# Optimization experiments

Hardware: AMD Instinct MI355X
Metric: run time of the kernel (lower is better)

## Reference

```python
import jax, jax.numpy as jnp
import numpy as np

V = 4096      # num codes (vocab)
D = 128       # embedding dim
K = 3         # diffusion scales
H = 4         # attn heads
FF = 128      # ff hidden
L = 2         # attn layers
NVIS = 8192   # visits
MAXC = 32     # max codes per visit
PAD = 0


def logmap0(x):
    # Poincare ball (c=1) log map at origin: artanh(||x||) * x / ||x||
    eps = 1e-7
    norm = jnp.linalg.norm(x, axis=-1, keepdims=True)
    norm_c = jnp.clip(norm, eps, 1.0 - 1e-5)
    return jnp.arctanh(norm_c) * x / jnp.maximum(norm, eps)


def layer_norm(x, g, b, eps=1e-5):
    m = jnp.mean(x, axis=-1, keepdims=True)
    v = jnp.mean((x - m) ** 2, axis=-1, keepdims=True)
    return (x - m) * jax.lax.rsqrt(v + eps) * g + b


def attn_block(x, Wqkv, bqkv, Wo, bo, W1, b1, W2, b2, g1, be1, g2, be2):
    # x: [V, D] (batch of 1, squeezed)
    hd = D // H
    qkv = x @ Wqkv.T + bqkv                      # [V, 3D]
    q, k, v = jnp.split(qkv, 3, axis=-1)
    q = q.reshape(V, H, hd)
    k = k.reshape(V, H, hd)
    v = v.reshape(V, H, hd)
    scores = jnp.einsum('shd,thd->hst', q, k) / np.sqrt(hd).astype(x.dtype)
    a = jax.nn.softmax(scores, axis=-1)          # [H, V, V]
    o = jnp.einsum('hst,thd->shd', a, v).reshape(V, D)
    attn_out = o @ Wo.T + bo
    x = layer_norm(x + attn_out, g1, be1)
    ff = jax.nn.gelu(x @ W1.T + b1) @ W2.T + b2
    return layer_norm(x + ff, g2, be2)


def setup_inputs() -> dict:
    key = jax.random.key(0)
    ks = jax.random.split(key, 20)
    inp = {}
    inp['visits'] = jax.random.randint(ks[0], (NVIS, MAXC), 0, V)
    # hyperbolic points inside unit ball
    inp['X_hyp'] = jax.random.normal(ks[1], (V, D), jnp.float32) * 0.01
    inp['kernels'] = jax.random.normal(ks[2], (K, V, V), jnp.float32) / V
    inp['proj_W'] = jax.random.normal(ks[3], (D, K * D), jnp.float32) * 0.05
    inp['proj_b'] = jnp.zeros((D,), jnp.float32)
    s = 0.05
    inp['Wqkv'] = jax.random.normal(ks[4], (L, 3 * D, D), jnp.float32) * s
    inp['bqkv'] = jnp.zeros((L, 3 * D), jnp.float32)
    inp['Wo'] = jax.random.normal(ks[5], (L, D, D), jnp.float32) * s
    inp['bo'] = jnp.zeros((L, D), jnp.float32)
    inp['W1'] = jax.random.normal(ks[6], (L, FF, D), jnp.float32) * s
    inp['b1'] = jnp.zeros((L, FF), jnp.float32)
    inp['W2'] = jax.random.normal(ks[7], (L, D, FF), jnp.float32) * s
    inp['b2'] = jnp.zeros((L, D), jnp.float32)
    inp['ln1_g'] = jnp.ones((L, D), jnp.float32)
    inp['ln1_b'] = jnp.zeros((L, D), jnp.float32)
    inp['ln2_g'] = jnp.ones((L, D), jnp.float32)
    inp['ln2_b'] = jnp.zeros((L, D), jnp.float32)
    return inp


def reference(visits, X_hyp, kernels, proj_W, proj_b, Wqkv, bqkv, Wo, bo,
              W1, b1, W2, b2, ln1_g, ln1_b, ln2_g, ln2_b):
    # ---- hyperbolic graph diffusion ----
    Z0 = logmap0(X_hyp)                              # [V, D]
    Z_scales = jnp.einsum('kuv,vd->ukd', kernels, Z0)  # [V, K, D]
    Z_cat = Z_scales.reshape(V, K * D)
    H_ = Z_cat @ proj_W.T + proj_b                   # [V, D]
    # ---- global self-attention stack ----
    for l in range(L):
        H_ = attn_block(H_, Wqkv[l], bqkv[l], Wo[l], bo[l],
                        W1[l], b1[l], W2[l], b2[l],
                        ln1_g[l], ln1_b[l], ln2_g[l], ln2_b[l])
    # ---- per-visit masked mean pooling (segment mean) ----
    mask = (visits != PAD)                           # [NVIS, MAXC]
    gathered = H_[visits] * mask[..., None]          # [NVIS, MAXC, D]
    cnt = jnp.sum(mask, axis=-1, keepdims=True).astype(H_.dtype)
    summed = jnp.sum(gathered, axis=1)               # [NVIS, D]
    return jnp.where(cnt > 0, summed / jnp.maximum(cnt, 1.0), 0.0)
```

## Files before the change

### kernel.cpp

```cpp
#include <hip/hip_runtime.h>
#include <hip/hip_bf16.h>
#include <math.h>

#define VN 4096
#define DIM 128
#define KS 3
#define NH 4
#define HD 32
#define NVIS 8192
#define MAXC 32
#define KTOT (KS*VN)

typedef unsigned short u16;
typedef __attribute__((ext_vector_type(8))) short short8;
typedef __attribute__((ext_vector_type(4))) float f32x4;

__device__ __forceinline__ u16 f2b(float f){
  union { float f; unsigned u; } c; c.f = f;
  unsigned u = c.u;
  return (u16)((u + 0x7fffu + ((u >> 16) & 1u)) >> 16);
}
__device__ __forceinline__ float b2f(u16 x){
  union { float f; unsigned u; } c; c.u = ((unsigned)x) << 16; return c.f;
}
#define MFMA16(a,b,c) __builtin_amdgcn_mfma_f32_16x16x32_bf16((a),(b),(c),0,0,0)

__global__ __launch_bounds__(256) void k_logmap(const float* __restrict__ xh, u16* __restrict__ z0){
  __shared__ float xs[64][132];
  __shared__ float part[4][64];
  __shared__ float sscale[64];
  int t = threadIdx.x;
  int v0 = blockIdx.x * 64;
  #pragma unroll
  for(int i=0;i<8;i++){
    int id = t + 256*i; int e = id*4; int r = e>>7; int c = e&127;
    float4 u = *(const float4*)&xh[(size_t)(v0+r)*DIM + c];
    xs[r][c+0]=u.x; xs[r][c+1]=u.y; xs[r][c+2]=u.z; xs[r][c+3]=u.w;
  }
  __syncthreads();
  int r = t & 63, q = t >> 6;
  float p = 0.f;
  #pragma unroll
  for(int c=0;c<32;c++){ float x = xs[r][q*32+c]; p += x*x; }
  part[q][r] = p;
  __syncthreads();
  if(t < 64){
    float ss = part[0][t]+part[1][t]+part[2][t]+part[3][t];
    float n = sqrtf(ss);
    float nc = fminf(fmaxf(n, 1e-7f), 1.0f - 1e-5f);
    sscale[t] = atanhf(nc) / fmaxf(n, 1e-7f);
  }
  __syncthreads();
  #pragma unroll
  for(int i=0;i<8;i++){
    int id = t + 256*i; int e = id*4; int rr = e>>7; int cc = e&127;
    float s = sscale[rr];
    ushort4 o;
    o.x = f2b(xs[rr][cc+0]*s); o.y = f2b(xs[rr][cc+1]*s);
    o.z = f2b(xs[rr][cc+2]*s); o.w = f2b(xs[rr][cc+3]*s);
    *(ushort4*)&z0[(size_t)(v0+rr)*DIM + cc] = o;
  }
}

template<bool AF32, bool BF32>
__device__ __forceinline__ void gemm_k128_t(const void* __restrict__ Agv, int lda,
                                            const void* __restrict__ Bgv, int ldb,
                                            u16* As, u16* Bs, f32x4 (&acc)[2][8]){
  int t = threadIdx.x;
  int w=t>>6, lane=t&63, l15=lane&15, quad=lane>>4;
  #pragma unroll
  for(int s=0;s<2;s++)
    #pragma unroll
    for(int n=0;n<8;n++) acc[s][n] = (f32x4){0.f,0.f,0.f,0.f};
  #pragma unroll
  for(int step=0; step<2; step++){
    int kb = step*64;
    __syncthreads();
    #pragma unroll
    for(int i=0;i<4;i++){
      int id = t + 256*i; int row = id>>3, c8 = id&7;
      if(AF32){
        const float* Ag = (const float*)Agv;
        float4 f0 = *(const float4*)&Ag[(size_t)row*lda + kb + c8*8];
        float4 f1 = *(const float4*)&Ag[(size_t)row*lda + kb + c8*8 + 4];
        ushort4 p0 = { f2b(f0.x), f2b(f0.y), f2b(f0.z), f2b(f0.w) };
        ushort4 p1 = { f2b(f1.x), f2b(f1.y), f2b(f1.z), f2b(f1.w) };
        *(ushort4*)&As[row*72 + c8*8]     = p0;
        *(ushort4*)&As[row*72 + c8*8 + 4] = p1;
      } else {
        const u16* Ag = (const u16*)Agv;
        *(uint4*)&As[row*72 + c8*8] = *(const uint4*)&Ag[(size_t)row*lda + kb + c8*8];
      }
      if(BF32){
        const float* Bg = (const float*)Bgv;
        float4 f0 = *(const float4*)&Bg[(size_t)row*ldb + kb + c8*8];
        float4 f1 = *(const float4*)&Bg[(size_t)row*ldb + kb + c8*8 + 4];
        ushort4 p0 = { f2b(f0.x), f2b(f0.y), f2b(f0.z), f2b(f0.w) };
        ushort4 p1 = { f2b(f1.x), f2b(f1.y), f2b(f1.z), f2b(f1.w) };
        *(ushort4*)&Bs[row*72 + c8*8]     = p0;
        *(ushort4*)&Bs[row*72 + c8*8 + 4] = p1;
      } else {
        const u16* Bg = (const u16*)Bgv;
        *(uint4*)&Bs[row*72 + c8*8] = *(const uint4*)&Bg[(size_t)row*ldb + kb + c8*8];
      }
    }
    __syncthreads();
    #pragma unroll
    for(int ks=0; ks<2; ks++){
      short8 a[2], b[8];
      #pragma unroll
      for(int s=0;s<2;s++) a[s] = *(short8*)&As[(w*32+s*16+l15)*72 + (ks*4+quad)*8];
      #pragma unroll
      for(int n=0;n<8;n++)  b[n] = *(short8*)&Bs[(n*16+l15)*72 + (ks*4+quad)*8];
      #pragma unroll
      for(int s=0;s<2;s++)
        #pragma unroll
        for(int n=0;n<8;n++) acc[s][n] = MFMA16(a[s], b[n], acc[s][n]);
    }
  }
}

__global__ __launch_bounds__(256) void k_gproj(const float* __restrict__ projW, const u16* __restrict__ z0,
                                               u16* __restrict__ gbuf){
  __shared__ u16 As[128*72], Bs[128*72];
  int kb = blockIdx.x >> 5, vt = blockIdx.x & 31;
  f32x4 acc[2][8];
  gemm_k128_t<true,false>(projW + kb*128, 3*DIM, z0 + (size_t)vt*128*DIM, DIM, As, Bs, acc);
  int t=threadIdx.x, w=t>>6, lane=t&63, l15=lane&15, quad=lane>>4;
  #pragma unroll
  for(int s=0;s<2;s++)
    #pragma unroll
    for(int n=0;n<8;n++)
      #pragma unroll
      for(int rg=0;rg<4;rg++){
        int d = w*32 + s*16 + quad*4 + rg;
        int v = vt*128 + n*16 + l15;
        gbuf[(size_t)(d*KS + kb)*VN + v] = f2b(acc[s][n][rg]);
      }
}

__global__ __launch_bounds__(256) void k_diff(const float* __restrict__ kers, const u16* __restrict__ gbuf,
                                              u16* __restrict__ hpart){
  __shared__ u16 As[128*72], Bs[128*72];
  int t = threadIdx.x;
  int mt = blockIdx.x & 31;
  int sl = blockIdx.x >> 5;
  int w=t>>6, lane=t&63, l15=lane&15, quad=lane>>4;
  f32x4 acc[2][8];
  #pragma unroll
  for(int s=0;s<2;s++)
    #pragma unroll
    for(int n=0;n<8;n++) acc[s][n] = (f32x4){0.f,0.f,0.f,0.f};
  int k0 = sl * 768;
  for(int step=0; step<12; step++){
    int kk = k0 + step*64;
    int kout = kk >> 12; int vv = kk & 4095;
    __syncthreads();
    #pragma unroll
    for(int i=0;i<4;i++){
      int id = t + 256*i; int row = id>>3, c8 = id&7;
      const float* ap = &kers[((size_t)kout<<24) + (size_t)(mt*128+row)*VN + vv + c8*8];
      float4 f0 = *(const float4*)ap;
      float4 f1 = *(const float4*)(ap+4);
      ushort4 p0 = { f2b(f0.x), f2b(f0.y), f2b(f0.z), f2b(f0.w) };
      ushort4 p1 = { f2b(f1.x), f2b(f1.y), f2b(f1.z), f2b(f1.w) };
      *(ushort4*)&As[row*72 + c8*8]     = p0;
      *(ushort4*)&As[row*72 + c8*8 + 4] = p1;
      *(uint4*)&Bs[row*72 + c8*8] = *(const uint4*)&gbuf[(size_t)row*KTOT + kk + c8*8];
    }
    __syncthreads();
    #pragma unroll
    for(int ks=0; ks<2; ks++){
      short8 a[2], b[8];
      #pragma unroll
      for(int s=0;s<2;s++) a[s] = *(short8*)&As[(w*32+s*16+l15)*72 + (ks*4+quad)*8];
      #pragma unroll
      for(int n=0;n<8;n++)  b[n] = *(short8*)&Bs[(n*16+l15)*72 + (ks*4+quad)*8];
      #pragma unroll
      for(int s=0;s<2;s++)
        #pragma unroll
        for(int n=0;n<8;n++) acc[s][n] = MFMA16(a[s], b[n], acc[s][n]);
    }
  }
  u16* dst = hpart + ((size_t)blockIdx.x << 14);
  #pragma unroll
  for(int s=0;s<2;s++)
    #pragma unroll
    for(int n=0;n<8;n++)
      #pragma unroll
      for(int rg=0;rg<4;rg++)
        dst[(w*32+s*16+quad*4+rg)*128 + n*16 + l15] = f2b(acc[s][n][rg]);
}

__global__ __launch_bounds__(256) void k_hreduce(const u16* __restrict__ hpart, const float* __restrict__ pb,
                                                 float* __restrict__ h0){
  int idx = blockIdx.x*256 + threadIdx.x;
  #pragma unroll
  for(int j=0;j<4;j++){
    int e = j*131072 + idx;
    float v = pb[e & 127];
    #pragma unroll
    for(int sl=0; sl<16; sl++) v += b2f(hpart[((size_t)sl<<19) + e]);
    h0[e] = v;
  }
}

template<bool AF32>
__global__ __launch_bounds__(256) void k_qkv(const void* __restrict__ xb, const float* __restrict__ Wq,
                                             const float* __restrict__ bq, u16* __restrict__ outq){
  __shared__ u16 As[128*72], Bs[128*72];
  int mt = blockIdx.x & 31, ntile = blockIdx.x >> 5;
  f32x4 acc[2][8];
  const void* Ap = AF32 ? (const void*)((const float*)xb + (size_t)mt*128*DIM)
                        : (const void*)((const u16*)xb + (size_t)mt*128*DIM);
  gemm_k128_t<AF32,true>(Ap, DIM, Wq + (size_t)ntile*128*DIM, DIM, As, Bs, acc);
  int t=threadIdx.x, w=t>>6, lane=t&63, l15=lane&15, quad=lane>>4;
  #pragma unroll
  for(int s=0;s<2;s++)
    #pragma unroll
    for(int n=0;n<8;n++)
      #pragma unroll
      for(int rg=0;rg<4;rg++){
        int row = mt*128 + w*32 + s*16 + quad*4 + rg;
        int col = ntile*128 + n*16 + l15;
        outq[(size_t)row*(3*DIM) + col] = f2b(acc[s][n][rg] + bq[col]);
      }
}

__global__ __launch_bounds__(256) void k_attn(const u16* __restrict__ qkv, float* __restrict__ opart,
                                              float* __restrict__ mlpart){
  __shared__ u16 Qs[64*40];
  __shared__ u16 Ksh[2][128*40];
  __shared__ u16 Vt[2][32*136];
  __shared__ u16 Ps[4*16*136];
  int t=threadIdx.x;
  int b = blockIdx.x;
  int h = b>>7, qt = (b>>1)&63, half = b&1;
  int w=t>>6, lane=t&63, l15=lane&15, quad=lane>>4;
  { int r = t>>2, c = t&3;
    *(uint4*)&Qs[r*40 + c*8] = *(const uint4*)&qkv[(size_t)(qt*64+r)*(3*DIM) + h*HD + c*8];
  }
  int skey = t>>2, sc4 = t&3;
  uint4 kreg[2], vreg[2];
  #pragma unroll
  for(int i=0;i<2;i++){
    int key = skey + 64*i;
    kreg[i] = *(const uint4*)&qkv[(size_t)((size_t)(half*16)*128+key)*(3*DIM) + DIM + h*HD + sc4*8];
    vreg[i] = *(const uint4*)&qkv[(size_t)((size_t)(half*16)*128+key)*(3*DIM) + 2*DIM + h*HD + sc4*8];
  }
  #pragma unroll
  for(int i=0;i<2;i++){
    int key = skey + 64*i;
    *(uint4*)&Ksh[0][key*40 + sc4*8] = kreg[i];
    u16 tmp[8]; *(uint4*)tmp = vreg[i];
    #pragma unroll
    for(int j=0;j<8;j++) Vt[0][(sc4*8+j)*136 + key] = tmp[j];
  }
  __syncthreads();
  short8 aq = *(short8*)&Qs[(w*16+l15)*40 + quad*8];
  f32x4 oacc[2]; oacc[0]=(f32x4){0.f,0.f,0.f,0.f}; oacc[1]=(f32x4){0.f,0.f,0.f,0.f};
  float mrun[4], lrun[4];
  #pragma unroll
  for(int rg=0;rg<4;rg++){ mrun[rg] = -INFINITY; lrun[rg] = 0.f; }
  const float sc = 0.17677669529663687f;
  for(int kti=0;kti<16;kti++){
    int cur = kti&1;
    if(kti<15){
      int kt = half*16 + kti + 1;
      #pragma unroll
      for(int i=0;i<2;i++){
        int key = skey + 64*i;
        kreg[i] = *(const uint4*)&qkv[(size_t)(kt*128+key)*(3*DIM) + DIM + h*HD + sc4*8];
        vreg[i] = *(const uint4*)&qkv[(size_t)(kt*128+key)*(3*DIM) + 2*DIM + h*HD + sc4*8];
      }
    }
    f32x4 s[8];
    #pragma unroll
    for(int n=0;n<8;n++)
      s[n] = MFMA16(aq, *(short8*)&Ksh[cur][(n*16+l15)*40 + quad*8], ((f32x4){0.f,0.f,0.f,0.f}));
    float mx[4];
    #pragma unroll
    for(int rg=0;rg<4;rg++){
      float m = -INFINITY;
      #pragma unroll
      for(int n=0;n<8;n++) m = fmaxf(m, s[n][rg]);
      #pragma unroll
      for(int off=1;off<16;off<<=1) m = fmaxf(m, __shfl_xor(m, off, 64));
      mx[rg] = m;
    }
    float alpha[4], rs[4];
    #pragma unroll
    for(int rg=0;rg<4;rg++){
      float mn = fmaxf(mrun[rg], mx[rg]);
      alpha[rg] = __expf(sc*(mrun[rg] - mn));
      mrun[rg] = mn; rs[rg] = 0.f;
    }
    #pragma unroll
    for(int n=0;n<8;n++)
      #pragma unroll
      for(int rg=0;rg<4;rg++){
        float p = __expf(sc*(s[n][rg] - mrun[rg]));
        s[n][rg] = p; rs[rg] += p;
      }
    #pragma unroll
    for(int rg=0;rg<4;rg++){
      #pragma unroll
      for(int off=1;off<16;off<<=1) rs[rg] += __shfl_xor(rs[rg], off, 64);
      lrun[rg] = lrun[rg]*alpha[rg] + rs[rg];
      oacc[0][rg] *= alpha[rg]; oacc[1][rg] *= alpha[rg];
    }
    #pragma unroll
    for(int n=0;n<8;n++)
      #pragma unroll
      for(int rg=0;rg<4;rg++)
        Ps[w*16*136 + (quad*4+rg)*136 + n*16 + l15] = f2b(s[n][rg]);
    #pragma unroll
    for(int kt2=0;kt2<4;kt2++){
      short8 ap = *(short8*)&Ps[w*16*136 + l15*136 + kt2*32 + quad*8];
      #pragma unroll
      for(int n2=0;n2<2;n2++)
        oacc[n2] = MFMA16(ap, *(short8*)&Vt[cur][(n2*16+l15)*136 + kt2*32 + quad*8], oacc[n2]);
    }
    if(kti<15){
      #pragma unroll
      for(int i=0;i<2;i++){
        int key = skey + 64*i;
        *(uint4*)&Ksh[cur^1][key*40 + sc4*8] = kreg[i];
        u16 tmp[8]; *(uint4*)tmp = vreg[i];
        #pragma unroll
        for(int j=0;j<8;j++) Vt[cur^1][(sc4*8+j)*136 + key] = tmp[j];
      }
    }
    __syncthreads();
  }
  float* op = opart + ((size_t)b << 11);
  #pragma unroll
  for(int n2=0;n2<2;n2++)
    #pragma unroll
    for(int rg=0;rg<4;rg++)
      op[(w*16+quad*4+rg)*32 + n2*16 + l15] = oacc[n2][rg];
  if(l15 == 0){
    float* ml = mlpart + ((size_t)b << 7);
    #pragma unroll
    for(int rg=0;rg<4;rg++){
      int r = w*16 + quad*4 + rg;
      ml[r] = sc*mrun[rg]; ml[64 + r] = lrun[rg];
    }
  }
}

__global__ __launch_bounds__(256) void k_oprojln(const float* __restrict__ opart, const float* __restrict__ mlpart,
                                                 const float* __restrict__ W,
                                                 const float* __restrict__ bias, const float* __restrict__ resf,
                                                 const float* __restrict__ g, const float* __restrict__ bb,
                                                 float* __restrict__ outf, u16* __restrict__ outb){
  __shared__ u16 As[128*72], Bs[128*72];
  int mt = blockIdx.x;
  int t=threadIdx.x, w=t>>6, lane=t&63, l15=lane&15, quad=lane>>4;
  f32x4 acc[2][8];
  #pragma unroll
  for(int s=0;s<2;s++)
    #pragma unroll
    for(int n=0;n<8;n++) acc[s][n] = (f32x4){0.f,0.f,0.f,0.f};
  #pragma unroll
  for(int step=0; step<2; step++){
    int kb = step*64;
    __syncthreads();
    #pragma unroll
    for(int i=0;i<4;i++){
      int id = t + 256*i; int row = id>>3, c8 = id&7;
      int col = kb + c8*8;
      int hh = col>>5, c0 = col&31;
      int grow = mt*128 + row;
      int hq = hh*64 + (grow>>6);
      int rr = grow & 63;
      const float* o0  = opart  + ((size_t)(hq*2)   << 11);
      const float* o1  = opart  + ((size_t)(hq*2+1) << 11);
      const float* ml0 = mlpart + ((size_t)(hq*2)   << 7);
      const float* ml1 = mlpart + ((size_t)(hq*2+1) << 7);
      float m0 = ml0[rr], l0 = ml0[64+rr], m1 = ml1[rr], l1 = ml1[64+rr];
      float m = fmaxf(m0, m1);
      float w0 = __expf(m0 - m), w1 = __expf(m1 - m);
      float inv = 1.f / (l0*w0 + l1*w1);
      float4 a0 = *(const float4*)&o0[rr*32 + c0];
      float4 a1 = *(const float4*)&o0[rr*32 + c0 + 4];
      float4 c0v = *(const float4*)&o1[rr*32 + c0];
      float4 c1v = *(const float4*)&o1[rr*32 + c0 + 4];
      ushort4 p0 = { f2b((a0.x*w0+c0v.x*w1)*inv), f2b((a0.y*w0+c0v.y*w1)*inv),
                     f2b((a0.z*w0+c0v.z*w1)*inv), f2b((a0.w*w0+c0v.w*w1)*inv) };
      ushort4 p1 = { f2b((a1.x*w0+c1v.x*w1)*inv), f2b((a1.y*w0+c1v.y*w1)*inv),
                     f2b((a1.z*w0+c1v.z*w1)*inv), f2b((a1.w*w0+c1v.w*w1)*inv) };
      *(ushort4*)&As[row*72 + c8*8]     = p0;
      *(ushort4*)&As[row*72 + c8*8 + 4] = p1;
      float4 f0 = *(const float4*)&W[(size_t)row*DIM + kb + c8*8];
      float4 f1 = *(const float4*)&W[(size_t)row*DIM + kb + c8*8 + 4];
      ushort4 q0 = { f2b(f0.x), f2b(f0.y), f2b(f0.z), f2b(f0.w) };
      ushort4 q1 = { f2b(f1.x), f2b(f1.y), f2b(f1.z), f2b(f1.w) };
      *(ushort4*)&Bs[row*72 + c8*8]     = q0;
      *(ushort4*)&Bs[row*72 + c8*8 + 4] = q1;
    }
    __syncthreads();
    #pragma unroll
    for(int ks=0; ks<2; ks++){
      short8 a[2], b[8];
      #pragma unroll
      for(int s=0;s<2;s++) a[s] = *(short8*)&As[(w*32+s*16+l15)*72 + (ks*4+quad)*8];
      #pragma unroll
      for(int n=0;n<8;n++)  b[n] = *(short8*)&Bs[(n*16+l15)*72 + (ks*4+quad)*8];
      #pragma unroll
      for(int s=0;s<2;s++)
        #pragma unroll
        for(int n=0;n<8;n++) acc[s][n] = MFMA16(a[s], b[n], acc[s][n]);
    }
  }
  #pragma unroll
  for(int s=0;s<2;s++)
    #pragma unroll
    for(int n=0;n<8;n++)
      #pragma unroll
      for(int rg=0;rg<4;rg++){
        int row = mt*128 + w*32 + s*16 + quad*4 + rg;
        int col = n*16 + l15;
        acc[s][n][rg] += bias[col] + resf[(size_t)row*DIM + col];
      }
  #pragma unroll
  for(int s=0;s<2;s++)
    #pragma unroll
    for(int rg=0;rg<4;rg++){
      float a=0.f, bsum=0.f;
      #pragma unroll
      for(int n=0;n<8;n++){ float x = acc[s][n][rg]; a += x; bsum += x*x; }
      #pragma unroll
      for(int off=1;off<16;off<<=1){ a += __shfl_xor(a, off, 64); bsum += __shfl_xor(bsum, off, 64); }
      float mean = a*(1.f/128.f);
      float var  = bsum*(1.f/128.f) - mean*mean;
      float rstd = rsqrtf(var + 1e-5f);
      #pragma unroll
      for(int n=0;n<8;n++){
        int row = mt*128 + w*32 + s*16 + quad*4 + rg;
        int col = n*16 + l15;
        float y = (acc[s][n][rg] - mean)*rstd*g[col] + bb[col];
        outf[(size_t)row*DIM + col] = y;
        outb[(size_t)row*DIM + col] = f2b(y);
      }
    }
}

__global__ __launch_bounds__(256) void k_projln(const u16* __restrict__ Ab, const float* __restrict__ W,
                                                const float* __restrict__ bias, const float* __restrict__ resf,
                                                const float* __restrict__ g, const float* __restrict__ bb,
                                                float* __restrict__ outf, u16* __restrict__ outb){
  __shared__ u16 As[128*72], Bs[128*72];
  int mt = blockIdx.x;
  f32x4 acc[2][8];
  gemm_k128_t<false,true>(Ab + (size_t)mt*128*DIM, DIM, W, DIM, As, Bs, acc);
  int t=threadIdx.x, w=t>>6, lane=t&63, l15=lane&15, quad=lane>>4;
  #pragma unroll
  for(int s=0;s<2;s++)
    #pragma unroll
    for(int n=0;n<8;n++)
      #pragma unroll
      for(int rg=0;rg<4;rg++){
        int row = mt*128 + w*32 + s*16 + quad*4 + rg;
        int col = n*16 + l15;
        acc[s][n][rg] += bias[col] + resf[(size_t)row*DIM + col];
      }
  #pragma unroll
  for(int s=0;s<2;s++)
    #pragma unroll
    for(int rg=0;rg<4;rg++){
      float a=0.f, bsum=0.f;
      #pragma unroll
      for(int n=0;n<8;n++){ float x = acc[s][n][rg]; a += x; bsum += x*x; }
      #pragma unroll
      for(int off=1;off<16;off<<=1){ a += __shfl_xor(a, off, 64); bsum += __shfl_xor(bsum, off, 64); }
      float mean = a*(1.f/128.f);
      float var  = bsum*(1.f/128.f) - mean*mean;
      float rstd = rsqrtf(var + 1e-5f);
      #pragma unroll
      for(int n=0;n<8;n++){
        int row = mt*128 + w*32 + s*16 + quad*4 + rg;
        int col = n*16 + l15;
        float y = (acc[s][n][rg] - mean)*rstd*g[col] + bb[col];
        outf[(size_t)row*DIM + col] = y;
        outb[(size_t)row*DIM + col] = f2b(y);
      }
    }
}

__global__ __launch_bounds__(256) void k_ff1(const u16* __restrict__ Ab, const float* __restrict__ W,
                                             const float* __restrict__ bias, u16* __restrict__ outb){
  __shared__ u16 As[128*72], Bs[128*72];
  int mt = blockIdx.x;
  f32x4 acc[2][8];
  gemm_k128_t<false,true>(Ab + (size_t)mt*128*DIM, DIM, W, DIM, As, Bs, acc);
  int t=threadIdx.x, w=t>>6, lane=t&63, l15=lane&15, quad=lane>>4;
  #pragma unroll
  for(int s=0;s<2;s++)
    #pragma unroll
    for(int n=0;n<8;n++)
      #pragma unroll
      for(int rg=0;rg<4;rg++){
        int row = mt*128 + w*32 + s*16 + quad*4 + rg;
        int col = n*16 + l15;
        float v = acc[s][n][rg] + bias[col];
        float z = 0.7978845608028654f*(v + 0.044715f*v*v*v);
        float e = __expf(2.f*z);
        float th = 1.f - 2.f/(e + 1.f);
        outb[(size_t)row*DIM + col] = f2b(0.5f*v*(1.f + th));
      }
}

__global__ __launch_bounds__(256) void k_pool(const int* __restrict__ visits, const float* __restrict__ xf,
                                              float* __restrict__ out){
  int t = threadIdx.x;
  int vis = blockIdx.x*2 + (t>>7);
  int col = t & 127;
  float s = 0.f; int cnt = 0;
  #pragma unroll
  for(int j=0;j<MAXC;j++){
    int idx = visits[vis*MAXC + j];
    if(idx != 0){ s += xf[(size_t)idx*DIM + col]; cnt++; }
  }
  float r = (cnt > 0) ? s/(float)cnt : 0.f;
  out[(size_t)vis*DIM + col] = r;
}

extern "C" void kernel_launch(void* const* d_in, const int* in_sizes, int n_in,
                              void* d_out, int out_size, void* d_ws, size_t ws_size,
                              hipStream_t stream){
  (void)in_sizes; (void)n_in; (void)out_size; (void)ws_size;
  const int*   visits = (const int*)d_in[0];
  const float* xhyp  = (const float*)d_in[1];
  const float* kers  = (const float*)d_in[2];
  const float* projW = (const float*)d_in[3];
  const float* projb = (const float*)d_in[4];
  const float* Wqkv  = (const float*)d_in[5];
  const float* bqkv  = (const float*)d_in[6];
  const float* Wo    = (const float*)d_in[7];
  const float* bo    = (const float*)d_in[8];
  const float* W1    = (const float*)d_in[9];
  const float* b1    = (const float*)d_in[10];
  const float* W2    = (const float*)d_in[11];
  const float* b2    = (const float*)d_in[12];
  const float* g1    = (const float*)d_in[13];
  const float* be1   = (const float*)d_in[14];
  const float* g2    = (const float*)d_in[15];
  const float* be2   = (const float*)d_in[16];

  char* ws = (char*)d_ws;
  u16*   z0    = (u16*)(ws);
  u16*   gbuf  = (u16*)(ws + (1u<<20));
  float* h0    = (float*)(ws + (4u<<20));
  u16*   qkvb  = (u16*)(ws + (7u<<20));
  float* ln1f  = (float*)(ws + (11u<<20));
  u16*   ln1b  = (u16*)(ws + (13u<<20));
  u16*   ffa   = (u16*)(ws + (14u<<20));
  float* x1f   = (float*)(ws + (15u<<20));
  u16*   x1b   = (u16*)(ws + (17u<<20));
  float* x2f   = (float*)(ws + (18u<<20));
  u16*   x2b   = (u16*)(ws + (20u<<20));
  u16*   hpart = (u16*)(ws + (21u<<20));
  float* opart = (float*)(ws + (53u<<20));
  float* mlprt = (float*)(ws + (57u<<20));

  k_logmap<<<64,256,0,stream>>>(xhyp, z0);
  k_gproj<<<96,256,0,stream>>>(projW, z0, gbuf);
  k_diff<<<512,256,0,stream>>>(kers, gbuf, hpart);
  k_hreduce<<<512,256,0,stream>>>(hpart, projb, h0);

  const void* curA = (const void*)h0; bool af32 = true;
  const float* curf = h0;
  float* outfs[2] = {x1f, x2f}; u16* outbs[2] = {x1b, x2b};
  for(int l=0;l<2;l++){
    if(af32) k_qkv<true ><<<96,256,0,stream>>>(curA, Wqkv + (size_t)l*3*DIM*DIM, bqkv + (size_t)l*3*DIM, qkvb);
    else     k_qkv<false><<<96,256,0,stream>>>(curA, Wqkv + (size_t)l*3*DIM*DIM, bqkv + (size_t)l*3*DIM, qkvb);
    k_attn<<<512,256,0,stream>>>(qkvb, opart, mlprt);
    k_oprojln<<<32,256,0,stream>>>(opart, mlprt, Wo + (size_t)l*DIM*DIM, bo + (size_t)l*DIM, curf,
                                   g1 + (size_t)l*DIM, be1 + (size_t)l*DIM, ln1f, ln1b);
    k_ff1<<<32,256,0,stream>>>(ln1b, W1 + (size_t)l*DIM*DIM, b1 + (size_t)l*DIM, ffa);
    k_projln<<<32,256,0,stream>>>(ffa, W2 + (size_t)l*DIM*DIM, b2 + (size_t)l*DIM, ln1f,
                                  g2 + (size_t)l*DIM, be2 + (size_t)l*DIM, outfs[l], outbs[l]);
    curA = (const void*)outbs[l]; af32 = false; curf = outfs[l];
  }
  k_pool<<<4096,256,0,stream>>>(visits, curf, (float*)d_out);
}
```

Measured before the change: 589.5 us.

## Fuse out-projection, LayerNorm and FFN into one tail kernel per layer

```diff
diff --git a/kernel.cpp b/kernel.cpp
--- a/kernel.cpp
+++ b/kernel.cpp
@@ -193,7 +193,7 @@
 }
 
 __global__ __launch_bounds__(256) void k_hreduce(const u16* __restrict__ hpart, const float* __restrict__ pb,
-                                                 float* __restrict__ h0){
+                                                 float* __restrict__ h0, u16* __restrict__ h0b){
   int idx = blockIdx.x*256 + threadIdx.x;
   #pragma unroll
   for(int j=0;j<4;j++){
@@ -201,19 +201,16 @@
     float v = pb[e & 127];
     #pragma unroll
     for(int sl=0; sl<16; sl++) v += b2f(hpart[((size_t)sl<<19) + e]);
-    h0[e] = v;
-  }
-}
-
-template<bool AF32>
-__global__ __launch_bounds__(256) void k_qkv(const void* __restrict__ xb, const float* __restrict__ Wq,
+    h0[e] = v; h0b[e] = f2b(v);
+  }
+}
+
+__global__ __launch_bounds__(256) void k_qkv(const u16* __restrict__ xb, const float* __restrict__ Wq,
                                              const float* __restrict__ bq, u16* __restrict__ outq){
   __shared__ u16 As[128*72], Bs[128*72];
   int mt = blockIdx.x & 31, ntile = blockIdx.x >> 5;
   f32x4 acc[2][8];
-  const void* Ap = AF32 ? (const void*)((const float*)xb + (size_t)mt*128*DIM)
-                        : (const void*)((const u16*)xb + (size_t)mt*128*DIM);
-  gemm_k128_t<AF32,true>(Ap, DIM, Wq + (size_t)ntile*128*DIM, DIM, As, Bs, acc);
+  gemm_k128_t<false,true>(xb + (size_t)mt*128*DIM, DIM, Wq + (size_t)ntile*128*DIM, DIM, As, Bs, acc);
   int t=threadIdx.x, w=t>>6, lane=t&63, l15=lane&15, quad=lane>>4;
   #pragma unroll
   for(int s=0;s<2;s++)
@@ -349,12 +346,16 @@
   }
 }
 
-__global__ __launch_bounds__(256) void k_oprojln(const float* __restrict__ opart, const float* __restrict__ mlpart,
-                                                 const float* __restrict__ W,
-                                                 const float* __restrict__ bias, const float* __restrict__ resf,
-                                                 const float* __restrict__ g, const float* __restrict__ bb,
-                                                 float* __restrict__ outf, u16* __restrict__ outb){
-  __shared__ u16 As[128*72], Bs[128*72];
+__global__ __launch_bounds__(256) void k_tail(const float* __restrict__ opart, const float* __restrict__ mlpart,
+                                              const float* __restrict__ Wo, const float* __restrict__ bo,
+                                              const float* __restrict__ resf,
+                                              const float* __restrict__ g1, const float* __restrict__ be1,
+                                              const float* __restrict__ W1, const float* __restrict__ b1,
+                                              const float* __restrict__ W2, const float* __restrict__ b2,
+                                              const float* __restrict__ g2, const float* __restrict__ be2,
+                                              float* __restrict__ outf, u16* __restrict__ outb){
+  __shared__ u16 Af[128*136];
+  __shared__ u16 Bf[128*136];
   int mt = blockIdx.x;
   int t=threadIdx.x, w=t>>6, lane=t&63, l15=lane&15, quad=lane>>4;
   f32x4 acc[2][8];
@@ -390,29 +391,30 @@
                      f2b((a0.z*w0+c0v.z*w1)*inv), f2b((a0.w*w0+c0v.w*w1)*inv) };
       ushort4 p1 = { f2b((a1.x*w0+c1v.x*w1)*inv), f2b((a1.y*w0+c1v.y*w1)*inv),
                      f2b((a1.z*w0+c1v.z*w1)*inv), f2b((a1.w*w0+c1v.w*w1)*inv) };
-      *(ushort4*)&As[row*72 + c8*8]     = p0;
-      *(ushort4*)&As[row*72 + c8*8 + 4] = p1;
-      float4 f0 = *(const float4*)&W[(size_t)row*DIM + kb + c8*8];
-      float4 f1 = *(const float4*)&W[(size_t)row*DIM + kb + c8*8 + 4];
+      *(ushort4*)&Af[row*136 + col]     = p0;
+      *(ushort4*)&Af[row*136 + col + 4] = p1;
+      float4 f0 = *(const float4*)&Wo[(size_t)row*DIM + col];
+      float4 f1 = *(const float4*)&Wo[(size_t)row*DIM + col + 4];
       ushort4 q0 = { f2b(f0.x), f2b(f0.y), f2b(f0.z), f2b(f0.w) };
       ushort4 q1 = { f2b(f1.x), f2b(f1.y), f2b(f1.z), f2b(f1.w) };
-      *(ushort4*)&Bs[row*72 + c8*8]     = q0;
-      *(ushort4*)&Bs[row*72 + c8*8 + 4] = q1;
+      *(ushort4*)&Bf[row*136 + col]     = q0;
+      *(ushort4*)&Bf[row*136 + col + 4] = q1;
     }
     __syncthreads();
     #pragma unroll
     for(int ks=0; ks<2; ks++){
       short8 a[2], b[8];
       #pragma unroll
-      for(int s=0;s<2;s++) a[s] = *(short8*)&As[(w*32+s*16+l15)*72 + (ks*4+quad)*8];
-      #pragma unroll
-      for(int n=0;n<8;n++)  b[n] = *(short8*)&Bs[(n*16+l15)*72 + (ks*4+quad)*8];
+      for(int s=0;s<2;s++) a[s] = *(short8*)&Af[(w*32+s*16+l15)*136 + kb + (ks*4+quad)*8];
+      #pragma unroll
+      for(int n=0;n<8;n++)  b[n] = *(short8*)&Bf[(n*16+l15)*136 + kb + (ks*4+quad)*8];
       #pragma unroll
       for(int s=0;s<2;s++)
         #pragma unroll
         for(int n=0;n<8;n++) acc[s][n] = MFMA16(a[s], b[n], acc[s][n]);
     }
   }
+  f32x4 res1[2][8];
   #pragma unroll
   for(int s=0;s<2;s++)
     #pragma unroll
@@ -421,7 +423,7 @@
       for(int rg=0;rg<4;rg++){
         int row = mt*128 + w*32 + s*16 + quad*4 + rg;
         int col = n*16 + l15;
-        acc[s][n][rg] += bias[col] + resf[(size_t)row*DIM + col];
+        acc[s][n][rg] += bo[col] + resf[(size_t)row*DIM + col];
       }
   #pragma unroll
   for(int s=0;s<2;s++)
@@ -437,33 +439,97 @@
       float rstd = rsqrtf(var + 1e-5f);
       #pragma unroll
       for(int n=0;n<8;n++){
-        int row = mt*128 + w*32 + s*16 + quad*4 + rg;
         int col = n*16 + l15;
-        float y = (acc[s][n][rg] - mean)*rstd*g[col] + bb[col];
-        outf[(size_t)row*DIM + col] = y;
-        outb[(size_t)row*DIM + col] = f2b(y);
-      }
-    }
-}
-
-__global__ __launch_bounds__(256) void k_projln(const u16* __restrict__ Ab, const float* __restrict__ W,
-                                                const float* __restrict__ bias, const float* __restrict__ resf,
-                                                const float* __restrict__ g, const float* __restrict__ bb,
-                                                float* __restrict__ outf, u16* __restrict__ outb){
-  __shared__ u16 As[128*72], Bs[128*72];
-  int mt = blockIdx.x;
-  f32x4 acc[2][8];
-  gemm_k128_t<false,true>(Ab + (size_t)mt*128*DIM, DIM, W, DIM, As, Bs, acc);
-  int t=threadIdx.x, w=t>>6, lane=t&63, l15=lane&15, quad=lane>>4;
+        float y = (acc[s][n][rg] - mean)*rstd*g1[col] + be1[col];
+        res1[s][n][rg] = y;
+        Af[(w*32+s*16+quad*4+rg)*136 + col] = f2b(y);
+      }
+    }
+  __syncthreads();
+  #pragma unroll
+  for(int i=0;i<8;i++){
+    int id = t + 256*i; int row = id>>4, c16 = id&15; int col = c16*8;
+    float4 f0 = *(const float4*)&W1[(size_t)row*DIM + col];
+    float4 f1 = *(const float4*)&W1[(size_t)row*DIM + col + 4];
+    ushort4 q0 = { f2b(f0.x), f2b(f0.y), f2b(f0.z), f2b(f0.w) };
+    ushort4 q1 = { f2b(f1.x), f2b(f1.y), f2b(f1.z), f2b(f1.w) };
+    *(ushort4*)&Bf[row*136 + col]     = q0;
+    *(ushort4*)&Bf[row*136 + col + 4] = q1;
+  }
+  __syncthreads();
+  #pragma unroll
+  for(int s=0;s<2;s++)
+    #pragma unroll
+    for(int n=0;n<8;n++) acc[s][n] = (f32x4){0.f,0.f,0.f,0.f};
+  #pragma unroll
+  for(int step=0; step<2; step++){
+    int kb = step*64;
+    #pragma unroll
+    for(int ks=0; ks<2; ks++){
+      short8 a[2], b[8];
+      #pragma unroll
+      for(int s=0;s<2;s++) a[s] = *(short8*)&Af[(w*32+s*16+l15)*136 + kb + (ks*4+quad)*8];
+      #pragma unroll
+      for(int n=0;n<8;n++)  b[n] = *(short8*)&Bf[(n*16+l15)*136 + kb + (ks*4+quad)*8];
+      #pragma unroll
+      for(int s=0;s<2;s++)
+        #pragma unroll
+        for(int n=0;n<8;n++) acc[s][n] = MFMA16(a[s], b[n], acc[s][n]);
+    }
+  }
   #pragma unroll
   for(int s=0;s<2;s++)
     #pragma unroll
     for(int n=0;n<8;n++)
       #pragma unroll
       for(int rg=0;rg<4;rg++){
-        int row = mt*128 + w*32 + s*16 + quad*4 + rg;
         int col = n*16 + l15;
-        acc[s][n][rg] += bias[col] + resf[(size_t)row*DIM + col];
+        float v = acc[s][n][rg] + b1[col];
+        float z = 0.7978845608028654f*(v + 0.044715f*v*v*v);
+        float e = __expf(2.f*z);
+        float th = 1.f - 2.f/(e + 1.f);
+        Af[(w*32+s*16+quad*4+rg)*136 + col] = f2b(0.5f*v*(1.f + th));
+      }
+  __syncthreads();
+  #pragma unroll
+  for(int i=0;i<8;i++){
+    int id = t + 256*i; int row = id>>4, c16 = id&15; int col = c16*8;
+    float4 f0 = *(const float4*)&W2[(size_t)row*DIM + col];
+    float4 f1 = *(const float4*)&W2[(size_t)row*DIM + col + 4];
+    ushort4 q0 = { f2b(f0.x), f2b(f0.y), f2b(f0.z), f2b(f0.w) };
+    ushort4 q1 = { f2b(f1.x), f2b(f1.y), f2b(f1.z), f2b(f1.w) };
+    *(ushort4*)&Bf[row*136 + col]     = q0;
+    *(ushort4*)&Bf[row*136 + col + 4] = q1;
+  }
+  __syncthreads();
+  #pragma unroll
+  for(int s=0;s<2;s++)
+    #pragma unroll
+    for(int n=0;n<8;n++) acc[s][n] = (f32x4){0.f,0.f,0.f,0.f};
+  #pragma unroll
+  for(int step=0; step<2; step++){
+    int kb = step*64;
+    #pragma unroll
+    for(int ks=0; ks<2; ks++){
+      short8 a[2], b[8];
+      #pragma unroll
+      for(int s=0;s<2;s++) a[s] = *(short8*)&Af[(w*32+s*16+l15)*136 + kb + (ks*4+quad)*8];
+      #pragma unroll
+      for(int n=0;n<8;n++)  b[n] = *(short8*)&Bf[(n*16+l15)*136 + kb + (ks*4+quad)*8];
+      #pragma unroll
+      for(int s=0;s<2;s++)
+        #pragma unroll
+        for(int n=0;n<8;n++) acc[s][n] = MFMA16(a[s], b[n], acc[s][n]);
+    }
+  }
+  #pragma unroll
+  for(int s=0;s<2;s++)
+    #pragma unroll
+    for(int n=0;n<8;n++)
+      #pragma unroll
+      for(int rg=0;rg<4;rg++){
+        int col = n*16 + l15;
+        acc[s][n][rg] += b2[col] + res1[s][n][rg];
       }
   #pragma unroll
   for(int s=0;s<2;s++)
@@ -481,37 +547,14 @@
       for(int n=0;n<8;n++){
         int row = mt*128 + w*32 + s*16 + quad*4 + rg;
         int col = n*16 + l15;
-        float y = (acc[s][n][rg] - mean)*rstd*g[col] + bb[col];
+        float y = (acc[s][n][rg] - mean)*rstd*g2[col] + be2[col];
         outf[(size_t)row*DIM + col] = y;
         outb[(size_t)row*DIM + col] = f2b(y);
       }
     }
 }
 
-__global__ __launch_bounds__(256) void k_ff1(const u16* __restrict__ Ab, const float* __restrict__ W,
-                                             const float* __restrict__ bias, u16* __restrict__ outb){
-  __shared__ u16 As[128*72], Bs[128*72];
-  int mt = blockIdx.x;
-  f32x4 acc[2][8];
-  gemm_k128_t<false,true>(Ab + (size_t)mt*128*DIM, DIM, W, DIM, As, Bs, acc);
-  int t=threadIdx.x, w=t>>6, lane=t&63, l15=lane&15, quad=lane>>4;
-  #pragma unroll
-  for(int s=0;s<2;s++)
-    #pragma unroll
-    for(int n=0;n<8;n++)
-      #pragma unroll
-      for(int rg=0;rg<4;rg++){
-        int row = mt*128 + w*32 + s*16 + quad*4 + rg;
-        int col = n*16 + l15;
-        float v = acc[s][n][rg] + bias[col];
-        float z = 0.7978845608028654f*(v + 0.044715f*v*v*v);
-        float e = __expf(2.f*z);
-        float th = 1.f - 2.f/(e + 1.f);
-        outb[(size_t)row*DIM + col] = f2b(0.5f*v*(1.f + th));
-      }
-}
-
-__global__ __launch_bounds__(256) void k_pool(const int* __restrict__ visits, const float* __restrict__ xf,
+__global__ __launch_bounds__(256) void k_pool(const int* __restrict__ visits, const u16* __restrict__ xb,
                                               float* __restrict__ out){
   int t = threadIdx.x;
   int vis = blockIdx.x*2 + (t>>7);
@@ -520,7 +563,7 @@
   #pragma unroll
   for(int j=0;j<MAXC;j++){
     int idx = visits[vis*MAXC + j];
-    if(idx != 0){ s += xf[(size_t)idx*DIM + col]; cnt++; }
+    if(idx != 0){ s += b2f(xb[(size_t)idx*DIM + col]); cnt++; }
   }
   float r = (cnt > 0) ? s/(float)cnt : 0.f;
   out[(size_t)vis*DIM + col] = r;
@@ -552,10 +595,8 @@
   u16*   z0    = (u16*)(ws);
   u16*   gbuf  = (u16*)(ws + (1u<<20));
   float* h0    = (float*)(ws + (4u<<20));
+  u16*   h0b   = (u16*)(ws + (6u<<20));
   u16*   qkvb  = (u16*)(ws + (7u<<20));
-  float* ln1f  = (float*)(ws + (11u<<20));
-  u16*   ln1b  = (u16*)(ws + (13u<<20));
-  u16*   ffa   = (u16*)(ws + (14u<<20));
   float* x1f   = (float*)(ws + (15u<<20));
   u16*   x1b   = (u16*)(ws + (17u<<20));
   float* x2f   = (float*)(ws + (18u<<20));
@@ -567,21 +608,21 @@
   k_logmap<<<64,256,0,stream>>>(xhyp, z0);
   k_gproj<<<96,256,0,stream>>>(projW, z0, gbuf);
   k_diff<<<512,256,0,stream>>>(kers, gbuf, hpart);
-  k_hreduce<<<512,256,0,stream>>>(hpart, projb, h0);
-
-  const void* curA = (const void*)h0; bool af32 = true;
-  const float* curf = h0;
+  k_hreduce<<<512,256,0,stream>>>(hpart, projb, h0, h0b);
+
+  const u16* curb = h0b; const float* curf = h0;
   float* outfs[2] = {x1f, x2f}; u16* outbs[2] = {x1b, x2b};
   for(int l=0;l<2;l++){
-    if(af32) k_qkv<true ><<<96,256,0,stream>>>(curA, Wqkv + (size_t)l*3*DIM*DIM, bqkv + (size_t)l*3*DIM, qkvb);
-    else     k_qkv<false><<<96,256,0,stream>>>(curA, Wqkv + (size_t)l*3*DIM*DIM, bqkv + (size_t)l*3*DIM, qkvb);
+    k_qkv<<<96,256,0,stream>>>(curb, Wqkv + (size_t)l*3*DIM*DIM, bqkv + (size_t)l*3*DIM, qkvb);
     k_attn<<<512,256,0,stream>>>(qkvb, opart, mlprt);
-    k_oprojln<<<32,256,0,stream>>>(opart, mlprt, Wo + (size_t)l*DIM*DIM, bo + (size_t)l*DIM, curf,
-                                   g1 + (size_t)l*DIM, be1 + (size_t)l*DIM, ln1f, ln1b);
-    k_ff1<<<32,256,0,stream>>>(ln1b, W1 + (size_t)l*DIM*DIM, b1 + (size_t)l*DIM, ffa);
-    k_projln<<<32,256,0,stream>>>(ffa, W2 + (size_t)l*DIM*DIM, b2 + (size_t)l*DIM, ln1f,
-                                  g2 + (size_t)l*DIM, be2 + (size_t)l*DIM, outfs[l], outbs[l]);
-    curA = (const void*)outbs[l]; af32 = false; curf = outfs[l];
-  }
-  k_pool<<<4096,256,0,stream>>>(visits, curf, (float*)d_out);
-}
+    k_tail<<<32,256,0,stream>>>(opart, mlprt,
+                                Wo + (size_t)l*DIM*DIM, bo + (size_t)l*DIM, curf,
+                                g1 + (size_t)l*DIM, be1 + (size_t)l*DIM,
+                                W1 + (size_t)l*DIM*DIM, b1 + (size_t)l*DIM,
+                                W2 + (size_t)l*DIM*DIM, b2 + (size_t)l*DIM,
+                                g2 + (size_t)l*DIM, be2 + (size_t)l*DIM,
+                                outfs[l], outbs[l]);
+    curb = outbs[l]; curf = outfs[l];
+  }
+  k_pool<<<4096,256,0,stream>>>(visits, curb, (float*)d_out);
+}
```

New measurement: 628.6 us. +6.6%, slower.
